# Kernel optimization log

Hardware: AMD Instinct MI355X
Metric: run time of the kernel (lower is better)

Reference implementation:

```python
import jax, jax.numpy as jnp
import numpy as np

HIDDEN = 2048
NUM_HEADS = 16
HEAD_DIM = HIDDEN // NUM_HEADS
HARMONICS = 64


def _holo_params(key, in_features, out_features, harmonics):
    kb, kp = jax.random.split(key)
    basis = jax.random.normal(kb, (harmonics, in_features), dtype=jnp.float32)
    basis = basis / jnp.linalg.norm(basis, axis=1, keepdims=True)  # F.normalize(p=2, dim=1)
    phase = jax.random.normal(kp, (out_features, harmonics), dtype=jnp.float32) * 0.1
    amp = jnp.ones((out_features, harmonics), dtype=jnp.float32) / np.sqrt(harmonics).astype(np.float32)
    return basis, phase, amp


def setup_inputs() -> dict:
    key = jax.random.key(0)
    ks = jax.random.split(key, 5)
    hidden_states = jax.random.normal(ks[0], (2, 2048, HIDDEN), dtype=jnp.float32)
    inp = {"hidden_states": hidden_states}
    for name, k in zip(("q", "k", "v", "o"), ks[1:]):
        basis, phase, amp = _holo_params(k, HIDDEN, HIDDEN, HARMONICS)
        inp[f"basis_{name}"] = basis
        inp[f"phase_{name}"] = phase
        inp[f"amp_{name}"] = amp
    return inp


def _holo_linear(x, basis, phase, amp):
    # resonance: (B,S,H) = x @ basis^T; modulated-sum == resonance @ (amp*cos(phase))^T
    resonance = jnp.einsum('bsd,hd->bsh', x, basis)
    w = amp * jnp.cos(phase)  # (out, harmonics)
    return jnp.einsum('bsh,oh->bso', resonance, w)


def reference(hidden_states, basis_q, phase_q, amp_q, basis_k, phase_k, amp_k,
              basis_v, phase_v, amp_v, basis_o, phase_o, amp_o):
    bsz, seq_len, _ = hidden_states.shape
    q = _holo_linear(hidden_states, basis_q, phase_q, amp_q)
    k = _holo_linear(hidden_states, basis_k, phase_k, amp_k)
    v = _holo_linear(hidden_states, basis_v, phase_v, amp_v)
    # (B, H, S, Dh)
    q = q.reshape(bsz, seq_len, NUM_HEADS, HEAD_DIM).transpose(0, 2, 1, 3)
    k = k.reshape(bsz, seq_len, NUM_HEADS, HEAD_DIM).transpose(0, 2, 1, 3)
    v = v.reshape(bsz, seq_len, NUM_HEADS, HEAD_DIM).transpose(0, 2, 1, 3)
    scale = 1.0 / np.sqrt(HEAD_DIM).astype(np.float32)
    scores = jnp.einsum('bhqd,bhkd->bhqk', q, k) * scale
    attn = jax.nn.softmax(scores, axis=-1)
    out = jnp.einsum('bhqk,bhkd->bhqd', attn, v)
    out = out.transpose(0, 2, 1, 3).reshape(bsz, seq_len, HIDDEN)
    return _holo_linear(out, basis_o, phase_o, amp_o)
```

## Files before the change

### kernel.cpp

```cpp
#include <hip/hip_runtime.h>
#include <hip/hip_bf16.h>
#include <math.h>

#define HIDDEN 2048
#define HARM   64
#define NHEADS 16
#define HDIM   128
#define SEQ    2048
#define BATCH  2
#define ROWS   (BATCH*SEQ)
#define RN     (ROWS*HARM)
#define PN     ((size_t)ROWS*HIDDEN)

using bf16x8 = __attribute__((ext_vector_type(8))) short;
using f32x16 = __attribute__((ext_vector_type(16))) float;

__device__ inline void split_bf(float a, ushort& hi, ushort& lo) {
  __hip_bfloat16 h = __float2bfloat16(a);
  float hf = __bfloat162float(h);
  __hip_bfloat16 l = __float2bfloat16(a - hf);
  union { __hip_bfloat16 b; ushort u; } c1, c2;
  c1.b = h; c2.b = l;
  hi = c1.u; lo = c2.u;
}

__global__ __launch_bounds__(256) void cast_x(
    const float* __restrict__ X, ushort* __restrict__ Xh, ushort* __restrict__ Xl) {
  size_t i = ((size_t)blockIdx.x * 256 + threadIdx.x) * 4;
  float4 v = *(const float4*)&X[i];
  ushort4 h, l;
  split_bf(v.x, h.x, l.x); split_bf(v.y, h.y, l.y);
  split_bf(v.z, h.z, l.z); split_bf(v.w, h.w, l.w);
  *(ushort4*)&Xh[i] = h;
  *(ushort4*)&Xl[i] = l;
}

__global__ __launch_bounds__(256) void cast_basis(
    const float* __restrict__ bq, const float* __restrict__ bk,
    const float* __restrict__ bv, const float* __restrict__ bo,
    ushort* __restrict__ Bh, ushort* __restrict__ Bl) {
  const int z = blockIdx.y;
  const float* S = (z == 0) ? bq : (z == 1) ? bk : (z == 2) ? bv : bo;
  size_t i = ((size_t)blockIdx.x * 256 + threadIdx.x) * 4;
  float4 v = *(const float4*)&S[i];
  ushort4 h, l;
  split_bf(v.x, h.x, l.x); split_bf(v.y, h.y, l.y);
  split_bf(v.z, h.z, l.z); split_bf(v.w, h.w, l.w);
  size_t o = (size_t)z * HARM * HIDDEN + i;
  *(ushort4*)&Bh[o] = h;
  *(ushort4*)&Bl[o] = l;
}

__global__ __launch_bounds__(256) void wt2_kernel(
    const float* __restrict__ pq, const float* __restrict__ aq,
    const float* __restrict__ pk, const float* __restrict__ ak,
    const float* __restrict__ pv, const float* __restrict__ av,
    const float* __restrict__ po, const float* __restrict__ ao,
    ushort* __restrict__ Wh, ushort* __restrict__ Wl) {
  int i = blockIdx.x * 256 + threadIdx.x;
  const int N = HIDDEN * HARM;
  int set = i / N, j = i - set * N;
  const float* p = (set == 0) ? pq : (set == 1) ? pk : (set == 2) ? pv : po;
  const float* a = (set == 0) ? aq : (set == 1) ? ak : (set == 2) ? av : ao;
  float wv = a[j] * cosf(p[j]);
  ushort h, l;
  split_bf(wv, h, l);
  size_t o = (size_t)set * N + j;
  Wh[o] = h; Wl[o] = l;
}

__global__ __launch_bounds__(256) void gemm_res(
    const ushort* __restrict__ Xh, const ushort* __restrict__ Xl,
    const ushort* __restrict__ Bh, const ushort* __restrict__ Bl,
    float* __restrict__ R0, float* __restrict__ R1, float* __restrict__ R2) {
  const int z = blockIdx.z;
  const ushort* Bhz = Bh + (size_t)z * HARM * HIDDEN;
  const ushort* Blz = Bl + (size_t)z * HARM * HIDDEN;
  float* Rp = (z == 0) ? R0 : (z == 1) ? R1 : R2;
  const int row0 = blockIdx.x * 64;
  const int kc = blockIdx.y;
  __shared__ __align__(16) ushort Xs[2][64][72];
  __shared__ __align__(16) ushort Bs[2][64][72];
  const int t = threadIdx.x;
  const int lane = t & 63, w = t >> 6;
  const int l31 = lane & 31, hh = lane >> 5;
  const int m0 = (w & 1) * 32, n0 = (w >> 1) * 32;
  const int srow = t >> 2;
  const int sc = (t & 3) * 16;
  f32x16 acc;
  #pragma unroll
  for (int j = 0; j < 16; ++j) acc[j] = 0.0f;

  const int kbase = kc * 512;
  for (int k0 = kbase; k0 < kbase + 512; k0 += 64) {
    const size_t xo = (size_t)(row0 + srow) * HIDDEN + k0 + sc;
    const size_t bo = (size_t)srow * HIDDEN + k0 + sc;
    *(uint4*)&Xs[0][srow][sc]     = *(const uint4*)&Xh[xo];
    *(uint4*)&Xs[0][srow][sc + 8] = *(const uint4*)&Xh[xo + 8];
    *(uint4*)&Xs[1][srow][sc]     = *(const uint4*)&Xl[xo];
    *(uint4*)&Xs[1][srow][sc + 8] = *(const uint4*)&Xl[xo + 8];
    *(uint4*)&Bs[0][srow][sc]     = *(const uint4*)&Bhz[bo];
    *(uint4*)&Bs[0][srow][sc + 8] = *(const uint4*)&Bhz[bo + 8];
    *(uint4*)&Bs[1][srow][sc]     = *(const uint4*)&Blz[bo];
    *(uint4*)&Bs[1][srow][sc + 8] = *(const uint4*)&Blz[bo + 8];
    __syncthreads();
    #pragma unroll
    for (int ks = 0; ks < 4; ++ks) {
      bf16x8 ah = *(const bf16x8*)&Xs[0][m0 + l31][ks * 16 + 8 * hh];
      bf16x8 al = *(const bf16x8*)&Xs[1][m0 + l31][ks * 16 + 8 * hh];
      bf16x8 bh = *(const bf16x8*)&Bs[0][n0 + l31][ks * 16 + 8 * hh];
      bf16x8 bl = *(const bf16x8*)&Bs[1][n0 + l31][ks * 16 + 8 * hh];
      acc = __builtin_amdgcn_mfma_f32_32x32x16_bf16(ah, bh, acc, 0, 0, 0);
      acc = __builtin_amdgcn_mfma_f32_32x32x16_bf16(al, bh, acc, 0, 0, 0);
      acc = __builtin_amdgcn_mfma_f32_32x32x16_bf16(ah, bl, acc, 0, 0, 0);
    }
    __syncthreads();
  }
  float* out = Rp + (size_t)kc * ROWS * HARM;
  #pragma unroll
  for (int r = 0; r < 16; ++r) {
    int mloc = (r & 3) + 8 * (r >> 2) + 4 * hh;
    out[(size_t)(row0 + m0 + mloc) * HARM + n0 + l31] = acc[r];
  }
}

__global__ __launch_bounds__(256) void gemm_proj(
    const float* __restrict__ Rp0, const float* __restrict__ Rp1,
    const float* __restrict__ Rp2,
    const ushort* __restrict__ Wh, const ushort* __restrict__ Wl,
    ushort* __restrict__ P0, ushort* __restrict__ P1, ushort* __restrict__ P2) {
  const int z = blockIdx.z;
  const float* Rp = (z == 0) ? Rp0 : (z == 1) ? Rp1 : Rp2;
  const ushort* Whz = Wh + (size_t)z * HIDDEN * HARM;
  const ushort* Wlz = Wl + (size_t)z * HIDDEN * HARM;
  ushort* P = (z == 0) ? P0 : (z == 1) ? P1 : P2;
  const int row0 = blockIdx.x * 32;
  const int col0 = blockIdx.y * 128;
  __shared__ __align__(16) ushort Rs[2][32][72];
  __shared__ __align__(16) ushort Ws[2][128][72];
  const int t = threadIdx.x;
  const int lane = t & 63, w = t >> 6;
  const int l31 = lane & 31, hh = lane >> 5;
  {
    const int r = t >> 3, h0 = (t & 7) * 8;
    const size_t o = (size_t)(row0 + r) * HARM + h0;
    #pragma unroll
    for (int e = 0; e < 8; ++e) {
      float v = Rp[o + e] + Rp[RN + o + e] + Rp[2 * (size_t)RN + o + e] +
                Rp[3 * (size_t)RN + o + e];
      ushort hi, lo;
      split_bf(v, hi, lo);
      Rs[0][r][h0 + e] = hi;
      Rs[1][r][h0 + e] = lo;
    }
  }
  #pragma unroll
  for (int i = 0; i < 4; ++i) {
    int idx = t + i * 256;
    int o = idx >> 3, c8 = (idx & 7) * 8;
    const size_t go = (size_t)(col0 + o) * HARM + c8;
    *(uint4*)&Ws[0][o][c8] = *(const uint4*)&Whz[go];
    *(uint4*)&Ws[1][o][c8] = *(const uint4*)&Wlz[go];
  }
  __syncthreads();
  const int n0 = w * 32;
  f32x16 acc;
  #pragma unroll
  for (int j = 0; j < 16; ++j) acc[j] = 0.0f;
  #pragma unroll
  for (int ks = 0; ks < 4; ++ks) {
    bf16x8 ah = *(const bf16x8*)&Rs[0][l31][ks * 16 + 8 * hh];
    bf16x8 al = *(const bf16x8*)&Rs[1][l31][ks * 16 + 8 * hh];
    bf16x8 bh = *(const bf16x8*)&Ws[0][n0 + l31][ks * 16 + 8 * hh];
    bf16x8 bl = *(const bf16x8*)&Ws[1][n0 + l31][ks * 16 + 8 * hh];
    acc = __builtin_amdgcn_mfma_f32_32x32x16_bf16(ah, bh, acc, 0, 0, 0);
    acc = __builtin_amdgcn_mfma_f32_32x32x16_bf16(al, bh, acc, 0, 0, 0);
    acc = __builtin_amdgcn_mfma_f32_32x32x16_bf16(ah, bl, acc, 0, 0, 0);
  }
  #pragma unroll
  for (int r = 0; r < 16; ++r) {
    int mloc = (r & 3) + 8 * (r >> 2) + 4 * hh;
    union { __hip_bfloat16 b; ushort u; } cv;
    cv.b = __float2bfloat16(acc[r]);
    P[(size_t)(row0 + mloc) * HIDDEN + col0 + n0 + l31] = cv.u;
  }
}

__global__ __launch_bounds__(256) void gemm_proj_f32(
    const float* __restrict__ Rp,
    const ushort* __restrict__ Whz, const ushort* __restrict__ Wlz,
    float* __restrict__ P) {
  const int row0 = blockIdx.x * 32;
  const int col0 = blockIdx.y * 128;
  __shared__ __align__(16) ushort Rs[2][32][72];
  __shared__ __align__(16) ushort Ws[2][128][72];
  const int t = threadIdx.x;
  const int lane = t & 63, w = t >> 6;
  const int l31 = lane & 31, hh = lane >> 5;
  {
    const int r = t >> 3, h0 = (t & 7) * 8;
    const size_t o = (size_t)(row0 + r) * HARM + h0;
    #pragma unroll
    for (int e = 0; e < 8; ++e) {
      float v = Rp[o + e] + Rp[RN + o + e] + Rp[2 * (size_t)RN + o + e] +
                Rp[3 * (size_t)RN + o + e];
      ushort hi, lo;
      split_bf(v, hi, lo);
      Rs[0][r][h0 + e] = hi;
      Rs[1][r][h0 + e] = lo;
    }
  }
  #pragma unroll
  for (int i = 0; i < 4; ++i) {
    int idx = t + i * 256;
    int o = idx >> 3, c8 = (idx & 7) * 8;
    const size_t go = (size_t)(col0 + o) * HARM + c8;
    *(uint4*)&Ws[0][o][c8] = *(const uint4*)&Whz[go];
    *(uint4*)&Ws[1][o][c8] = *(const uint4*)&Wlz[go];
  }
  __syncthreads();
  const int n0 = w * 32;
  f32x16 acc;
  #pragma unroll
  for (int j = 0; j < 16; ++j) acc[j] = 0.0f;
  #pragma unroll
  for (int ks = 0; ks < 4; ++ks) {
    bf16x8 ah = *(const bf16x8*)&Rs[0][l31][ks * 16 + 8 * hh];
    bf16x8 al = *(const bf16x8*)&Rs[1][l31][ks * 16 + 8 * hh];
    bf16x8 bh = *(const bf16x8*)&Ws[0][n0 + l31][ks * 16 + 8 * hh];
    bf16x8 bl = *(const bf16x8*)&Ws[1][n0 + l31][ks * 16 + 8 * hh];
    acc = __builtin_amdgcn_mfma_f32_32x32x16_bf16(ah, bh, acc, 0, 0, 0);
    acc = __builtin_amdgcn_mfma_f32_32x32x16_bf16(al, bh, acc, 0, 0, 0);
    acc = __builtin_amdgcn_mfma_f32_32x32x16_bf16(ah, bl, acc, 0, 0, 0);
  }
  #pragma unroll
  for (int r = 0; r < 16; ++r) {
    int mloc = (r & 3) + 8 * (r >> 2) + 4 * hh;
    P[(size_t)(row0 + mloc) * HIDDEN + col0 + n0 + l31] = acc[r];
  }
}

__global__ __launch_bounds__(256) void transpose_v(
    const ushort* __restrict__ S, ushort* __restrict__ D) {
  const int b = blockIdx.z;
  const int r0 = blockIdx.y * 32, c0 = blockIdx.x * 32;
  __shared__ ushort tile[32][33];
  const int t = threadIdx.x;
  const int r = t >> 3, cs = (t & 7) * 4;
  const ushort* Sb = S + (size_t)b * SEQ * HIDDEN;
  ushort* Db = D + (size_t)b * SEQ * HIDDEN;
  ushort4 v = *(const ushort4*)&Sb[(size_t)(r0 + r) * HIDDEN + c0 + cs];
  tile[r][cs] = v.x; tile[r][cs + 1] = v.y; tile[r][cs + 2] = v.z; tile[r][cs + 3] = v.w;
  __syncthreads();
  ushort4 o;
  o.x = tile[cs + 0][r]; o.y = tile[cs + 1][r];
  o.z = tile[cs + 2][r]; o.w = tile[cs + 3][r];
  *(ushort4*)&Db[(size_t)(c0 + r) * SEQ + r0 + cs] = o;
}

#define BQ 128
#define BK 64
#define KSTR 136
#define VSTR 72

__device__ inline unsigned pkbf(float a, float b) {
  __hip_bfloat162 h2 = __float22bfloat162_rn(make_float2(a, b));
  union { __hip_bfloat162 h; unsigned u; } cv; cv.h = h2; return cv.u;
}

__global__ __launch_bounds__(256, 2) void attn_mfma(
    const ushort* __restrict__ Qg, const ushort* __restrict__ Kg,
    const ushort* __restrict__ Vt, ushort* __restrict__ Oh,
    ushort* __restrict__ Ol) {
  __shared__ __align__(16) union SM {
    ushort q[BQ][KSTR];
    struct { ushort k[BK][KSTR]; ushort v[HDIM][VSTR]; } kv[2];
  } sm;
  const int t = threadIdx.x;
  const int bh = blockIdx.x & 31;
  const int qt = blockIdx.x >> 5;
  const int b = bh >> 4, h = bh & 15;
  const int q0 = qt * BQ;
  const int lane = t & 63;
  const int w = t >> 6;
  const int l31 = lane & 31;
  const int hh = lane >> 5;
  const bool hi = (hh != 0);
  const float SC2 = 0.08838834764831845f * 1.4426950408889634f;

  const int sk_key = t >> 4;
  const int sk_d0 = (t & 15) * 8;
  const int sv_d = t >> 3;
  const int sv_k = (t & 7) * 8;
  const size_t kbase = ((size_t)(b * SEQ)) * HIDDEN + h * HDIM;
  const size_t vbase = ((size_t)(b * SEQ + h * HDIM)) * SEQ;

  {
    const size_t gbase = ((size_t)(b * SEQ + q0)) * HIDDEN + h * HDIM;
    for (int p = 0; p < 8; ++p) {
      int row = p * 16 + sk_key;
      uint4 v = *(const uint4*)&Qg[gbase + (size_t)row * HIDDEN + sk_d0];
      *(uint4*)&sm.q[row][sk_d0] = v;
    }
  }
  __syncthreads();
  bf16x8 Qf[8];
  {
    const int qrow = w * 32 + l31;
    #pragma unroll
    for (int ks = 0; ks < 8; ++ks)
      Qf[ks] = *(const bf16x8*)&sm.q[qrow][ks * 16 + 8 * hh];
  }
  __syncthreads();

  float mrow = -1e30f, lsum = 0.0f;
  f32x16 Ot[4];
  #pragma unroll
  for (int i = 0; i < 4; ++i)
    #pragma unroll
    for (int j = 0; j < 16; ++j) Ot[i][j] = 0.0f;

  uint4 kp[4], vp[4];
  {
    const size_t gb = kbase;
    #pragma unroll
    for (int p = 0; p < 4; ++p)
      kp[p] = *(const uint4*)&Kg[gb + (size_t)(p * 16 + sk_key) * HIDDEN + sk_d0];
    #pragma unroll
    for (int p = 0; p < 4; ++p)
      vp[p] = *(const uint4*)&Vt[vbase + (size_t)(p * 32 + sv_d) * SEQ + sv_k];
    #pragma unroll
    for (int p = 0; p < 4; ++p)
      *(uint4*)&sm.kv[0].k[p * 16 + sk_key][sk_d0] = kp[p];
    #pragma unroll
    for (int p = 0; p < 4; ++p)
      *(uint4*)&sm.kv[0].v[p * 32 + sv_d][sv_k] = vp[p];
  }
  __syncthreads();

  for (int ci = 0; ci < 32; ++ci) {
    {
      const int cn = (ci < 31) ? ci + 1 : 31;
      const size_t gb = kbase + (size_t)(cn * BK) * HIDDEN;
      #pragma unroll
      for (int p = 0; p < 4; ++p)
        kp[p] = *(const uint4*)&Kg[gb + (size_t)(p * 16 + sk_key) * HIDDEN + sk_d0];
      const size_t vb = vbase + cn * BK;
      #pragma unroll
      for (int p = 0; p < 4; ++p)
        vp[p] = *(const uint4*)&Vt[vb + (size_t)(p * 32 + sv_d) * SEQ + sv_k];
    }
    const int cb = ci & 1;

    f32x16 C0, C1;
    #pragma unroll
    for (int j = 0; j < 16; ++j) { C0[j] = 0.0f; C1[j] = 0.0f; }
    #pragma unroll
    for (int ks = 0; ks < 8; ++ks) {
      bf16x8 a0 = *(const bf16x8*)&sm.kv[cb].k[l31][ks * 16 + 8 * hh];
      bf16x8 a1 = *(const bf16x8*)&sm.kv[cb].k[32 + l31][ks * 16 + 8 * hh];
      C0 = __builtin_amdgcn_mfma_f32_32x32x16_bf16(a0, Qf[ks], C0, 0, 0, 0);
      C1 = __builtin_amdgcn_mfma_f32_32x32x16_bf16(a1, Qf[ks], C1, 0, 0, 0);
    }

    float mxr = -1e30f;
    #pragma unroll
    for (int j = 0; j < 16; ++j) mxr = fmaxf(mxr, fmaxf(C0[j], C1[j]));
    mxr = fmaxf(mxr, __shfl_xor(mxr, 32));
    const float mnew = fmaxf(mrow, mxr * SC2);
    const float alpha = exp2f(mrow - mnew);
    float ssum = 0.0f;
    #pragma unroll
    for (int j = 0; j < 16; ++j) {
      float e0 = exp2f(fmaf(C0[j], SC2, -mnew));
      float e1 = exp2f(fmaf(C1[j], SC2, -mnew));
      C0[j] = e0; C1[j] = e1;
      ssum += e0 + e1;
    }
    ssum += __shfl_xor(ssum, 32);
    lsum = lsum * alpha + ssum;
    mrow = mnew;
    #pragma unroll
    for (int i = 0; i < 4; ++i)
      #pragma unroll
      for (int j = 0; j < 16; ++j) Ot[i][j] *= alpha;

    #pragma unroll
    for (int st = 0; st < 4; ++st) {
      const int eb = 8 * (st & 1);
      float o0, o1, o2, o3, g0, g1, g2, g3;
      if (st < 2) {
        o0 = hi ? C0[eb + 4] : C0[eb + 0]; o1 = hi ? C0[eb + 5] : C0[eb + 1];
        o2 = hi ? C0[eb + 6] : C0[eb + 2]; o3 = hi ? C0[eb + 7] : C0[eb + 3];
        g0 = hi ? C0[eb + 0] : C0[eb + 4]; g1 = hi ? C0[eb + 1] : C0[eb + 5];
        g2 = hi ? C0[eb + 2] : C0[eb + 6]; g3 = hi ? C0[eb + 3] : C0[eb + 7];
      } else {
        o0 = hi ? C1[eb + 4] : C1[eb + 0]; o1 = hi ? C1[eb + 5] : C1[eb + 1];
        o2 = hi ? C1[eb + 6] : C1[eb + 2]; o3 = hi ? C1[eb + 7] : C1[eb + 3];
        g0 = hi ? C1[eb + 0] : C1[eb + 4]; g1 = hi ? C1[eb + 1] : C1[eb + 5];
        g2 = hi ? C1[eb + 2] : C1[eb + 6]; g3 = hi ? C1[eb + 3] : C1[eb + 7];
      }
      unsigned so0 = pkbf(o0, o1), so1 = pkbf(o2, o3);
      unsigned sp0 = pkbf(g0, g1), sp1 = pkbf(g2, g3);
      unsigned r0 = (unsigned)__shfl_xor((int)sp0, 32);
      unsigned r1 = (unsigned)__shfl_xor((int)sp1, 32);
      union { unsigned u[4]; bf16x8 v; } cv;
      cv.u[0] = hi ? r0 : so0;
      cv.u[1] = hi ? r1 : so1;
      cv.u[2] = hi ? so0 : r0;
      cv.u[3] = hi ? so1 : r1;
      #pragma unroll
      for (int mt = 0; mt < 4; ++mt) {
        bf16x8 a2 = *(const bf16x8*)&sm.kv[cb].v[mt * 32 + l31][st * 16 + 8 * hh];
        Ot[mt] = __builtin_amdgcn_mfma_f32_32x32x16_bf16(a2, cv.v, Ot[mt], 0, 0, 0);
      }
    }

    {
      const int nb = cb ^ 1;
      #pragma unroll
      for (int p = 0; p < 4; ++p)
        *(uint4*)&sm.kv[nb].k[p * 16 + sk_key][sk_d0] = kp[p];
      #pragma unroll
      for (int p = 0; p < 4; ++p)
        *(uint4*)&sm.kv[nb].v[p * 32 + sv_d][sv_k] = vp[p];
    }
    __syncthreads();
  }

  const float inv = 1.0f / lsum;
  const int qrow = q0 + w * 32 + l31;
  const size_t ob = ((size_t)(b * SEQ + qrow)) * HIDDEN + h * HDIM;
  #pragma unroll
  for (int mt = 0; mt < 4; ++mt)
    #pragma unroll
    for (int g = 0; g < 4; ++g) {
      ushort4 hs, ls;
      split_bf(Ot[mt][4 * g + 0] * inv, hs.x, ls.x);
      split_bf(Ot[mt][4 * g + 1] * inv, hs.y, ls.y);
      split_bf(Ot[mt][4 * g + 2] * inv, hs.z, ls.z);
      split_bf(Ot[mt][4 * g + 3] * inv, hs.w, ls.w);
      const size_t off = ob + mt * 32 + 8 * g + 4 * hh;
      *(ushort4*)&Oh[off] = hs;
      *(ushort4*)&Ol[off] = ls;
    }
}

extern "C" void kernel_launch(void* const* d_in, const int* in_sizes, int n_in,
                              void* d_out, int out_size, void* d_ws, size_t ws_size,
                              hipStream_t stream) {
  (void)in_sizes; (void)n_in; (void)out_size; (void)ws_size;
  const float* X       = (const float*)d_in[0];
  const float* basis_q = (const float*)d_in[1];
  const float* phase_q = (const float*)d_in[2];
  const float* amp_q   = (const float*)d_in[3];
  const float* basis_k = (const float*)d_in[4];
  const float* phase_k = (const float*)d_in[5];
  const float* amp_k   = (const float*)d_in[6];
  const float* basis_v = (const float*)d_in[7];
  const float* phase_v = (const float*)d_in[8];
  const float* amp_v   = (const float*)d_in[9];
  const float* basis_o = (const float*)d_in[10];
  const float* phase_o = (const float*)d_in[11];
  const float* amp_o   = (const float*)d_in[12];

  const size_t WN = (size_t)HIDDEN * HARM;

  char* p = (char*)d_ws;
  ushort* Xhi = (ushort*)p; p += PN * 2;
  ushort* Xlo = (ushort*)p; p += PN * 2;
  ushort* Bhi = (ushort*)p; p += 4 * WN * 2;
  ushort* Blo = (ushort*)p; p += 4 * WN * 2;
  ushort* Whi = (ushort*)p; p += 4 * WN * 2;
  ushort* Wlo = (ushort*)p; p += 4 * WN * 2;
  float* Rqp = (float*)p; p += (size_t)4 * RN * 4;
  float* Rkp = (float*)p; p += (size_t)4 * RN * 4;
  float* Rvp = (float*)p; p += (size_t)4 * RN * 4;
  float* Rop = (float*)p; p += (size_t)4 * RN * 4;
  __hip_bfloat16* Qb = (__hip_bfloat16*)p; p += PN * 2;
  __hip_bfloat16* Kb = (__hip_bfloat16*)p; p += PN * 2;
  __hip_bfloat16* Vb = (__hip_bfloat16*)p; p += PN * 2;
  __hip_bfloat16* VtB = (__hip_bfloat16*)p; p += PN * 2;
  ushort* AOh = (ushort*)p; p += PN * 2;
  ushort* AOl = (ushort*)p; p += PN * 2;
  float* out = (float*)d_out;

  cast_x<<<8192, 256, 0, stream>>>(X, Xhi, Xlo);
  wt2_kernel<<<2048, 256, 0, stream>>>(phase_q, amp_q, phase_k, amp_k,
                                       phase_v, amp_v, phase_o, amp_o,
                                       Whi, Wlo);
  cast_basis<<<dim3(128, 4), 256, 0, stream>>>(basis_q, basis_k, basis_v, basis_o,
                                               Bhi, Blo);

  gemm_res<<<dim3(64, 4, 3), 256, 0, stream>>>(Xhi, Xlo, Bhi, Blo, Rqp, Rkp, Rvp);

  gemm_proj<<<dim3(128, 16, 3), 256, 0, stream>>>(
      Rqp, Rkp, Rvp, Whi, Wlo, (ushort*)Qb, (ushort*)Kb, (ushort*)Vb);

  transpose_v<<<dim3(HIDDEN / 32, SEQ / 32, BATCH), 256, 0, stream>>>(
      (const ushort*)Vb, (ushort*)VtB);

  attn_mfma<<<dim3((SEQ / BQ) * 32), 256, 0, stream>>>(
      (const ushort*)Qb, (const ushort*)Kb, (const ushort*)VtB, AOh, AOl);

  gemm_res<<<dim3(64, 4, 1), 256, 0, stream>>>(
      AOh, AOl, Bhi + 3 * WN, Blo + 3 * WN, Rop, Rop, Rop);

  gemm_proj_f32<<<dim3(128, 16), 256, 0, stream>>>(
      Rop, Whi + 3 * WN, Wlo + 3 * WN, out);
}
```

Measured before the change: 286.6 us.

## Merge prep casts into one kernel and fuse V transpose into projection

Combines the three preprocessing kernels (X split, weight cos, basis split) into a single launch with block-range dispatch. The V projection now writes its output already transposed, staging the tile through shared memory in a union with the GEMM buffers, so the separate transpose kernel and the intermediate V buffer go away. This is meant to cut launch overhead and one full round trip of V through global memory. In exchange the V branch adds an extra barrier and 64-byte strided stores.

```diff
diff --git a/kernel.cpp b/kernel.cpp
--- a/kernel.cpp
+++ b/kernel.cpp
@@ -24,49 +24,51 @@
   hi = c1.u; lo = c2.u;
 }
 
-__global__ __launch_bounds__(256) void cast_x(
-    const float* __restrict__ X, ushort* __restrict__ Xh, ushort* __restrict__ Xl) {
-  size_t i = ((size_t)blockIdx.x * 256 + threadIdx.x) * 4;
-  float4 v = *(const float4*)&X[i];
-  ushort4 h, l;
-  split_bf(v.x, h.x, l.x); split_bf(v.y, h.y, l.y);
-  split_bf(v.z, h.z, l.z); split_bf(v.w, h.w, l.w);
-  *(ushort4*)&Xh[i] = h;
-  *(ushort4*)&Xl[i] = l;
-}
-
-__global__ __launch_bounds__(256) void cast_basis(
-    const float* __restrict__ bq, const float* __restrict__ bk,
-    const float* __restrict__ bv, const float* __restrict__ bo,
-    ushort* __restrict__ Bh, ushort* __restrict__ Bl) {
-  const int z = blockIdx.y;
-  const float* S = (z == 0) ? bq : (z == 1) ? bk : (z == 2) ? bv : bo;
-  size_t i = ((size_t)blockIdx.x * 256 + threadIdx.x) * 4;
-  float4 v = *(const float4*)&S[i];
-  ushort4 h, l;
-  split_bf(v.x, h.x, l.x); split_bf(v.y, h.y, l.y);
-  split_bf(v.z, h.z, l.z); split_bf(v.w, h.w, l.w);
-  size_t o = (size_t)z * HARM * HIDDEN + i;
-  *(ushort4*)&Bh[o] = h;
-  *(ushort4*)&Bl[o] = l;
-}
-
-__global__ __launch_bounds__(256) void wt2_kernel(
+__global__ __launch_bounds__(256) void prep(
+    const float* __restrict__ X,
     const float* __restrict__ pq, const float* __restrict__ aq,
     const float* __restrict__ pk, const float* __restrict__ ak,
     const float* __restrict__ pv, const float* __restrict__ av,
     const float* __restrict__ po, const float* __restrict__ ao,
-    ushort* __restrict__ Wh, ushort* __restrict__ Wl) {
-  int i = blockIdx.x * 256 + threadIdx.x;
-  const int N = HIDDEN * HARM;
-  int set = i / N, j = i - set * N;
-  const float* p = (set == 0) ? pq : (set == 1) ? pk : (set == 2) ? pv : po;
-  const float* a = (set == 0) ? aq : (set == 1) ? ak : (set == 2) ? av : ao;
-  float wv = a[j] * cosf(p[j]);
-  ushort h, l;
-  split_bf(wv, h, l);
-  size_t o = (size_t)set * N + j;
-  Wh[o] = h; Wl[o] = l;
+    const float* __restrict__ bq, const float* __restrict__ bk,
+    const float* __restrict__ bv, const float* __restrict__ bo,
+    ushort* __restrict__ Xh, ushort* __restrict__ Xl,
+    ushort* __restrict__ Wh, ushort* __restrict__ Wl,
+    ushort* __restrict__ Bh, ushort* __restrict__ Bl) {
+  const int bid = blockIdx.x;
+  const int t = threadIdx.x;
+  if (bid < 8192) {
+    size_t i = ((size_t)bid * 256 + t) * 4;
+    float4 v = *(const float4*)&X[i];
+    ushort4 h, l;
+    split_bf(v.x, h.x, l.x); split_bf(v.y, h.y, l.y);
+    split_bf(v.z, h.z, l.z); split_bf(v.w, h.w, l.w);
+    *(ushort4*)&Xh[i] = h;
+    *(ushort4*)&Xl[i] = l;
+  } else if (bid < 10240) {
+    int i = (bid - 8192) * 256 + t;
+    const int N = HIDDEN * HARM;
+    int set = i / N, j = i - set * N;
+    const float* p = (set == 0) ? pq : (set == 1) ? pk : (set == 2) ? pv : po;
+    const float* a = (set == 0) ? aq : (set == 1) ? ak : (set == 2) ? av : ao;
+    float wv = a[j] * cosf(p[j]);
+    ushort h, l;
+    split_bf(wv, h, l);
+    size_t o = (size_t)set * N + j;
+    Wh[o] = h; Wl[o] = l;
+  } else {
+    int idx = bid - 10240;
+    int z = idx >> 7, xb = idx & 127;
+    const float* S = (z == 0) ? bq : (z == 1) ? bk : (z == 2) ? bv : bo;
+    size_t i = ((size_t)xb * 256 + t) * 4;
+    float4 v = *(const float4*)&S[i];
+    ushort4 h, l;
+    split_bf(v.x, h.x, l.x); split_bf(v.y, h.y, l.y);
+    split_bf(v.z, h.z, l.z); split_bf(v.w, h.w, l.w);
+    size_t o = (size_t)z * HARM * HIDDEN + i;
+    *(ushort4*)&Bh[o] = h;
+    *(ushort4*)&Bl[o] = l;
+  }
 }
 
 __global__ __launch_bounds__(256) void gemm_res(
@@ -128,16 +130,17 @@
     const float* __restrict__ Rp0, const float* __restrict__ Rp1,
     const float* __restrict__ Rp2,
     const ushort* __restrict__ Wh, const ushort* __restrict__ Wl,
-    ushort* __restrict__ P0, ushort* __restrict__ P1, ushort* __restrict__ P2) {
+    ushort* __restrict__ P0, ushort* __restrict__ P1, ushort* __restrict__ Vt) {
   const int z = blockIdx.z;
   const float* Rp = (z == 0) ? Rp0 : (z == 1) ? Rp1 : Rp2;
   const ushort* Whz = Wh + (size_t)z * HIDDEN * HARM;
   const ushort* Wlz = Wl + (size_t)z * HIDDEN * HARM;
-  ushort* P = (z == 0) ? P0 : (z == 1) ? P1 : P2;
   const int row0 = blockIdx.x * 32;
   const int col0 = blockIdx.y * 128;
-  __shared__ __align__(16) ushort Rs[2][32][72];
-  __shared__ __align__(16) ushort Ws[2][128][72];
+  __shared__ __align__(16) union PSM {
+    struct { ushort Rs[2][32][72]; ushort Ws[2][128][72]; } s;
+    ushort ct[128][36];
+  } sm;
   const int t = threadIdx.x;
   const int lane = t & 63, w = t >> 6;
   const int l31 = lane & 31, hh = lane >> 5;
@@ -150,8 +153,8 @@
                 Rp[3 * (size_t)RN + o + e];
       ushort hi, lo;
       split_bf(v, hi, lo);
-      Rs[0][r][h0 + e] = hi;
-      Rs[1][r][h0 + e] = lo;
+      sm.s.Rs[0][r][h0 + e] = hi;
+      sm.s.Rs[1][r][h0 + e] = lo;
     }
   }
   #pragma unroll
@@ -159,8 +162,8 @@
     int idx = t + i * 256;
     int o = idx >> 3, c8 = (idx & 7) * 8;
     const size_t go = (size_t)(col0 + o) * HARM + c8;
-    *(uint4*)&Ws[0][o][c8] = *(const uint4*)&Whz[go];
-    *(uint4*)&Ws[1][o][c8] = *(const uint4*)&Wlz[go];
+    *(uint4*)&sm.s.Ws[0][o][c8] = *(const uint4*)&Whz[go];
+    *(uint4*)&sm.s.Ws[1][o][c8] = *(const uint4*)&Wlz[go];
   }
   __syncthreads();
   const int n0 = w * 32;
@@ -169,20 +172,42 @@
   for (int j = 0; j < 16; ++j) acc[j] = 0.0f;
   #pragma unroll
   for (int ks = 0; ks < 4; ++ks) {
-    bf16x8 ah = *(const bf16x8*)&Rs[0][l31][ks * 16 + 8 * hh];
-    bf16x8 al = *(const bf16x8*)&Rs[1][l31][ks * 16 + 8 * hh];
-    bf16x8 bh = *(const bf16x8*)&Ws[0][n0 + l31][ks * 16 + 8 * hh];
-    bf16x8 bl = *(const bf16x8*)&Ws[1][n0 + l31][ks * 16 + 8 * hh];
+    bf16x8 ah = *(const bf16x8*)&sm.s.Rs[0][l31][ks * 16 + 8 * hh];
+    bf16x8 al = *(const bf16x8*)&sm.s.Rs[1][l31][ks * 16 + 8 * hh];
+    bf16x8 bh = *(const bf16x8*)&sm.s.Ws[0][n0 + l31][ks * 16 + 8 * hh];
+    bf16x8 bl = *(const bf16x8*)&sm.s.Ws[1][n0 + l31][ks * 16 + 8 * hh];
     acc = __builtin_amdgcn_mfma_f32_32x32x16_bf16(ah, bh, acc, 0, 0, 0);
     acc = __builtin_amdgcn_mfma_f32_32x32x16_bf16(al, bh, acc, 0, 0, 0);
     acc = __builtin_amdgcn_mfma_f32_32x32x16_bf16(ah, bl, acc, 0, 0, 0);
   }
-  #pragma unroll
-  for (int r = 0; r < 16; ++r) {
-    int mloc = (r & 3) + 8 * (r >> 2) + 4 * hh;
-    union { __hip_bfloat16 b; ushort u; } cv;
-    cv.b = __float2bfloat16(acc[r]);
-    P[(size_t)(row0 + mloc) * HIDDEN + col0 + n0 + l31] = cv.u;
+  if (z < 2) {
+    ushort* P = (z == 0) ? P0 : P1;
+    #pragma unroll
+    for (int r = 0; r < 16; ++r) {
+      int mloc = (r & 3) + 8 * (r >> 2) + 4 * hh;
+      union { __hip_bfloat16 b; ushort u; } cv;
+      cv.b = __float2bfloat16(acc[r]);
+      P[(size_t)(row0 + mloc) * HIDDEN + col0 + n0 + l31] = cv.u;
+    }
+  } else {
+    __syncthreads();
+    #pragma unroll
+    for (int r = 0; r < 16; ++r) {
+      int mloc = (r & 3) + 8 * (r >> 2) + 4 * hh;
+      union { __hip_bfloat16 b; ushort u; } cv;
+      cv.b = __float2bfloat16(acc[r]);
+      sm.ct[n0 + l31][mloc] = cv.u;
+    }
+    __syncthreads();
+    if (t < 128) {
+      const int batch = row0 >> 11;
+      const int tok0 = row0 & 2047;
+      ushort* dst = Vt + (size_t)batch * SEQ * HIDDEN +
+                    (size_t)(col0 + t) * SEQ + tok0;
+      #pragma unroll
+      for (int j = 0; j < 4; ++j)
+        *(uint4*)&dst[j * 8] = *(const uint4*)&sm.ct[t][j * 8];
+    }
   }
 }
 
@@ -238,24 +263,6 @@
     int mloc = (r & 3) + 8 * (r >> 2) + 4 * hh;
     P[(size_t)(row0 + mloc) * HIDDEN + col0 + n0 + l31] = acc[r];
   }
-}
-
-__global__ __launch_bounds__(256) void transpose_v(
-    const ushort* __restrict__ S, ushort* __restrict__ D) {
-  const int b = blockIdx.z;
-  const int r0 = blockIdx.y * 32, c0 = blockIdx.x * 32;
-  __shared__ ushort tile[32][33];
-  const int t = threadIdx.x;
-  const int r = t >> 3, cs = (t & 7) * 4;
-  const ushort* Sb = S + (size_t)b * SEQ * HIDDEN;
-  ushort* Db = D + (size_t)b * SEQ * HIDDEN;
-  ushort4 v = *(const ushort4*)&Sb[(size_t)(r0 + r) * HIDDEN + c0 + cs];
-  tile[r][cs] = v.x; tile[r][cs + 1] = v.y; tile[r][cs + 2] = v.z; tile[r][cs + 3] = v.w;
-  __syncthreads();
-  ushort4 o;
-  o.x = tile[cs + 0][r]; o.y = tile[cs + 1][r];
-  o.z = tile[cs + 2][r]; o.w = tile[cs + 3][r];
-  *(ushort4*)&Db[(size_t)(c0 + r) * SEQ + r0 + cs] = o;
 }
 
 #define BQ 128
@@ -479,26 +486,21 @@
   float* Rop = (float*)p; p += (size_t)4 * RN * 4;
   __hip_bfloat16* Qb = (__hip_bfloat16*)p; p += PN * 2;
   __hip_bfloat16* Kb = (__hip_bfloat16*)p; p += PN * 2;
-  __hip_bfloat16* Vb = (__hip_bfloat16*)p; p += PN * 2;
   __hip_bfloat16* VtB = (__hip_bfloat16*)p; p += PN * 2;
   ushort* AOh = (ushort*)p; p += PN * 2;
   ushort* AOl = (ushort*)p; p += PN * 2;
   float* out = (float*)d_out;
 
-  cast_x<<<8192, 256, 0, stream>>>(X, Xhi, Xlo);
-  wt2_kernel<<<2048, 256, 0, stream>>>(phase_q, amp_q, phase_k, amp_k,
-                                       phase_v, amp_v, phase_o, amp_o,
-                                       Whi, Wlo);
-  cast_basis<<<dim3(128, 4), 256, 0, stream>>>(basis_q, basis_k, basis_v, basis_o,
-                                               Bhi, Blo);
+  prep<<<10752, 256, 0, stream>>>(X,
+                                  phase_q, amp_q, phase_k, amp_k,
+                                  phase_v, amp_v, phase_o, amp_o,
+                                  basis_q, basis_k, basis_v, basis_o,
+                                  Xhi, Xlo, Whi, Wlo, Bhi, Blo);
 
   gemm_res<<<dim3(64, 4, 3), 256, 0, stream>>>(Xhi, Xlo, Bhi, Blo, Rqp, Rkp, Rvp);
 
   gemm_proj<<<dim3(128, 16, 3), 256, 0, stream>>>(
-      Rqp, Rkp, Rvp, Whi, Wlo, (ushort*)Qb, (ushort*)Kb, (ushort*)Vb);
-
-  transpose_v<<<dim3(HIDDEN / 32, SEQ / 32, BATCH), 256, 0, stream>>>(
-      (const ushort*)Vb, (ushort*)VtB);
+      Rqp, Rkp, Rvp, Whi, Wlo, (ushort*)Qb, (ushort*)Kb, (ushort*)VtB);
 
   attn_mfma<<<dim3((SEQ / BQ) * 32), 256, 0, stream>>>(
       (const ushort*)Qb, (const ushort*)Kb, (const ushort*)VtB, AOh, AOl);
```

After: 275.6 us. 1.04x faster.
